# Kernel optimization log

Measured on AMD Instinct MI355X. Metric: run time of the kernel, lower is better.

The kernel has to match this reference:

```python
import jax, jax.numpy as jnp
import numpy as np

B, S, E = 2, 2048, 4096
H, KVH, D = 32, 8, 128
GROUPS = H // KVH
MAX_POS = 4096
ROPE_THETA = 10000.0


def _rope_tables(max_pos, dim, theta):
    inv_freq = 1.0 / (theta ** (jnp.arange(0, dim, 2, dtype=jnp.float32) / dim))
    t = jnp.arange(max_pos, dtype=jnp.float32)
    freqs = jnp.einsum('i,j->ij', t, inv_freq)        # [max_pos, dim/2]
    emb = jnp.concatenate([freqs, freqs], axis=-1)    # [max_pos, dim]
    return jnp.cos(emb), jnp.sin(emb)


def _rotate_half(x):
    x1, x2 = x[..., : x.shape[-1] // 2], x[..., x.shape[-1] // 2:]
    return jnp.concatenate([-x2, x1], axis=-1)


def setup_inputs() -> dict:
    key = jax.random.key(0)
    ks = jax.random.split(key, 8)
    scale_w = 1.0 / np.sqrt(E)
    query = jax.random.normal(ks[0], (B, S, E), dtype=jnp.float32)
    k_in = jax.random.normal(ks[1], (B, S, E), dtype=jnp.float32)
    v_in = jax.random.normal(ks[2], (B, S, E), dtype=jnp.float32)
    position_ids = jnp.broadcast_to(jnp.arange(S, dtype=jnp.int64), (B, S))
    # causal mask: 1 where attending allowed, 0 elsewhere
    src_mask = jnp.tril(jnp.ones((S, S), dtype=jnp.int32))
    src_mask = jnp.broadcast_to(src_mask, (B, S, S))
    Wq = jax.random.normal(ks[3], (E, H * D), dtype=jnp.float32) * scale_w
    Wk = jax.random.normal(ks[4], (E, KVH * D), dtype=jnp.float32) * scale_w
    Wv = jax.random.normal(ks[5], (E, KVH * D), dtype=jnp.float32) * scale_w
    Wo = jax.random.normal(ks[6], (H * D, E), dtype=jnp.float32) * scale_w
    return {"query": query, "key": k_in, "value": v_in,
            "position_ids": position_ids, "src_mask": src_mask,
            "Wq": Wq, "Wk": Wk, "Wv": Wv, "Wo": Wo}


def reference(query, key, value, position_ids, src_mask, Wq, Wk, Wv, Wo):
    nb, q_len, _ = query.shape
    # projections -> [B, heads, S, D]
    q = (query @ Wq).reshape(nb, q_len, H, D).transpose(0, 2, 1, 3)
    k = (key @ Wk).reshape(nb, q_len, KVH, D).transpose(0, 2, 1, 3)
    v = (value @ Wv).reshape(nb, q_len, KVH, D).transpose(0, 2, 1, 3)
    # RoPE
    cos_t, sin_t = _rope_tables(MAX_POS, D, ROPE_THETA)
    cos = cos_t[position_ids][:, None]  # [B,1,S,D]
    sin = sin_t[position_ids][:, None]
    q = q * cos + _rotate_half(q) * sin
    k = k * cos + _rotate_half(k) * sin
    # repeat_kv (interleave groups) -> [B,H,S,D]
    k = jnp.repeat(k, GROUPS, axis=1)
    v = jnp.repeat(v, GROUPS, axis=1)
    # attention core
    scores = jnp.einsum('bhqd,bhkd->bhqk', q, k) / jnp.sqrt(jnp.float32(D))
    mask = src_mask[:, None]  # [B,1,S,S]
    scores = jnp.where(mask == 0, jnp.float32(-1e9), scores)
    attn = jax.nn.softmax(scores, axis=-1)
    x = jnp.einsum('bhqk,bhkd->bhqd', attn, v)
    x = x.transpose(0, 2, 1, 3).reshape(nb, q_len, H * D)
    return x @ Wo
```

## Files before the change

### kernel.cpp

```cpp
#include <hip/hip_runtime.h>
#include <stdint.h>

#define B_ 2
#define S_ 2048
#define E_ 4096
#define H_ 32
#define KVH_ 8
#define D_ 128

typedef __bf16 bf16_t;
typedef __bf16 bf16x8 __attribute__((ext_vector_type(8)));
typedef __bf16 bf16x4 __attribute__((ext_vector_type(4)));
typedef float f32x4 __attribute__((ext_vector_type(4)));

__device__ __forceinline__ void gl2lds16(const void* g, void* l) {
  __builtin_amdgcn_global_load_lds(
      (__attribute__((address_space(1))) void*)(uintptr_t)g,
      (__attribute__((address_space(3))) void*)(uint32_t)(uintptr_t)l,
      16, 0, 0);
}

__global__ void cvt_f32_bf16(const float* __restrict__ in, bf16_t* __restrict__ out, int n4) {
  int i = blockIdx.x * 256 + threadIdx.x;
  if (i < n4) {
    float4 v = ((const float4*)in)[i];
    bf16x4 o;
    o.x = (bf16_t)v.x; o.y = (bf16_t)v.y; o.z = (bf16_t)v.z; o.w = (bf16_t)v.w;
    ((bf16x4*)out)[i] = o;
  }
}

__global__ void transpose_cvt(const float* __restrict__ in, bf16_t* __restrict__ out,
                              int R, int C) {
  __shared__ float t[32][33];
  int r0 = blockIdx.y * 32, c0 = blockIdx.x * 32;
  int tx = threadIdx.x & 31, tg = threadIdx.x >> 5;
#pragma unroll
  for (int k = 0; k < 4; ++k) {
    int r = tg * 4 + k;
    t[r][tx] = in[(long)(r0 + r) * C + c0 + tx];
  }
  __syncthreads();
#pragma unroll
  for (int k = 0; k < 4; ++k) {
    int r = tg * 4 + k;
    out[(long)(c0 + r) * R + r0 + tx] = (bf16_t)t[tx][r];
  }
}

__global__ void transpose_v(const float* __restrict__ Vtmp, bf16_t* __restrict__ Vt) {
  __shared__ float t[32][33];
  int z = blockIdx.z, b = z >> 3, kv = z & 7;
  const float* in = Vtmp + (long)b * S_ * (KVH_ * D_) + kv * D_;
  bf16_t* out = Vt + ((long)(b * KVH_ + kv)) * D_ * S_;
  int s0 = blockIdx.y * 32, d0 = blockIdx.x * 32;
  int tx = threadIdx.x & 31, tg = threadIdx.x >> 5;
#pragma unroll
  for (int k = 0; k < 4; ++k) {
    int r = tg * 4 + k;
    t[r][tx] = in[(long)(s0 + r) * (KVH_ * D_) + d0 + tx];
  }
  __syncthreads();
#pragma unroll
  for (int k = 0; k < 4; ++k) {
    int r = tg * 4 + k;
    out[(long)(d0 + r) * S_ + s0 + tx] = (bf16_t)t[tx][r];
  }
}

__global__ void rope_cvt(const float* __restrict__ T, bf16_t* __restrict__ out,
                         const int* __restrict__ pos, int NH, float scale) {
  long idx = (long)blockIdx.x * 256 + threadIdx.x;
  int j = (int)(idx & 63);
  long t = idx >> 6;
  int s = (int)(t % S_); t /= S_;
  int nh = (int)(t % NH);
  int b = (int)(t / NH);
  long row = ((long)b * S_ + s) * ((long)NH * D_) + (long)nh * D_;
  float x1 = T[row + j];
  float x2 = T[row + j + 64];
  float p = (float)pos[(long)b * S_ + s];
  float inv = expf(-(float)j * (9.210340371976184f / 64.0f));
  float fr = p * inv;
  float c = cosf(fr), sn = sinf(fr);
  long ob = (((long)b * NH + nh) * S_ + s) * D_;
  out[ob + j]      = (bf16_t)((x1 * c - x2 * sn) * scale);
  out[ob + j + 64] = (bf16_t)((x2 * c + x1 * sn) * scale);
}

__global__ __launch_bounds__(256, 2) void gemm_bt(
    const bf16_t* __restrict__ A, const bf16_t* __restrict__ Bt,
    float* __restrict__ C, int M, int N, int K) {
  __shared__ bf16_t As[128 * 64];
  __shared__ bf16_t Bs[128 * 64];
  const int tid = threadIdx.x;
  const int lane = tid & 63;
  const int wave = tid >> 6;
  const int m0 = blockIdx.y * 128, n0 = blockIdx.x * 128;
  const int wm = (wave >> 1) * 64, wn = (wave & 1) * 64;
  const int ln = lane & 15, quad = lane >> 4;
  const int srow = lane >> 3;
  const int sg = lane & 7;

  f32x4 acc[4][4] = {};

  for (int kb = 0; kb < K; kb += 64) {
    __syncthreads();
#pragma unroll
    for (int it = 0; it < 4; ++it) {
      int c = wave * 4 + it;
      int row = c * 8 + srow;
      int g = sg ^ (row & 7);
      gl2lds16(A + (long)(m0 + row) * K + kb + g * 8, &As[c * 512 + lane * 8]);
      gl2lds16(Bt + (long)(n0 + row) * K + kb + g * 8, &Bs[c * 512 + lane * 8]);
    }
    __syncthreads();
#pragma unroll
    for (int ks = 0; ks < 2; ++ks) {
      bf16x8 af[4], bfr[4];
      const int go = ((ks * 4 + quad) ^ (ln & 7)) * 8;
#pragma unroll
      for (int i = 0; i < 4; ++i)
        af[i] = *(const bf16x8*)&As[(wm + i * 16 + ln) * 64 + go];
#pragma unroll
      for (int j = 0; j < 4; ++j)
        bfr[j] = *(const bf16x8*)&Bs[(wn + j * 16 + ln) * 64 + go];
#pragma unroll
      for (int i = 0; i < 4; ++i)
#pragma unroll
        for (int j = 0; j < 4; ++j)
          acc[i][j] = __builtin_amdgcn_mfma_f32_16x16x32_bf16(af[i], bfr[j], acc[i][j], 0, 0, 0);
    }
  }
#pragma unroll
  for (int i = 0; i < 4; ++i)
#pragma unroll
    for (int j = 0; j < 4; ++j)
#pragma unroll
      for (int r = 0; r < 4; ++r) {
        int m = m0 + wm + i * 16 + quad * 4 + r;
        int n = n0 + wn + j * 16 + ln;
        C[(long)m * N + n] = acc[i][j][r];
      }
}

__global__ __launch_bounds__(256, 1) void flash_attn(
    const bf16_t* __restrict__ Q, const bf16_t* __restrict__ Kr,
    const bf16_t* __restrict__ Vt, bf16_t* __restrict__ X) {
  __shared__ bf16_t Plds[4 * 32 * 128];
  const int tid = threadIdx.x, lane = tid & 63, wave = tid >> 6;
  const int ln = lane & 15, quad = lane >> 4;

  const int d = blockIdx.x;
  const int wid = (d & 7) * 128 + (d >> 3);
  const int qi = 15 - (wid & 15);
  const int h = (wid >> 4) & 31;
  const int b = wid >> 9;
  const int kv = h >> 2;
  const bf16_t* Kbase = Kr + (((long)b * KVH_ + kv) * S_) * D_;
  const bf16_t* Vbase = Vt + (((long)b * KVH_ + kv) * D_) * S_;
  bf16_t* Pw = &Plds[wave * 4096];

  bf16x8 aq[2][4];
  {
    const bf16_t* Qw = Q + (((long)b * H_ + h) * S_ + qi * 128 + wave * 32) * D_;
#pragma unroll
    for (int i = 0; i < 2; ++i)
#pragma unroll
      for (int ks = 0; ks < 4; ++ks)
        aq[i][ks] = *(const bf16x8*)(Qw + (i * 16 + ln) * D_ + ks * 32 + quad * 8);
  }

  f32x4 o_acc[2][8] = {};
  float m_cur[2][4], l_cur[2][4];
#pragma unroll
  for (int i = 0; i < 2; ++i)
#pragma unroll
    for (int r = 0; r < 4; ++r) { m_cur[i][r] = -__builtin_inff(); l_cur[i][r] = 0.f; }

  for (int jt = 0; jt <= qi; ++jt) {
    const bf16_t* Kt = Kbase + (long)jt * 128 * D_;

    f32x4 s_acc[2][8] = {};
#pragma unroll
    for (int ks = 0; ks < 4; ++ks) {
      bf16x8 bk[8];
#pragma unroll
      for (int j = 0; j < 8; ++j)
        bk[j] = *(const bf16x8*)(Kt + (long)(j * 16 + ln) * D_ + ks * 32 + quad * 8);
      __builtin_amdgcn_s_setprio(1);
#pragma unroll
      for (int i = 0; i < 2; ++i)
#pragma unroll
        for (int j = 0; j < 8; ++j)
          s_acc[i][j] = __builtin_amdgcn_mfma_f32_16x16x32_bf16(aq[i][ks], bk[j], s_acc[i][j], 0, 0, 0);
      __builtin_amdgcn_s_setprio(0);
    }

#pragma unroll
    for (int i = 0; i < 2; ++i) {
      float rmax[4];
#pragma unroll
      for (int r = 0; r < 4; ++r) rmax[r] = -__builtin_inff();
#pragma unroll
      for (int j = 0; j < 8; ++j)
#pragma unroll
        for (int r = 0; r < 4; ++r) {
          float v = s_acc[i][j][r];
          if (jt == qi) {
            int qrow = wave * 32 + i * 16 + quad * 4 + r;
            int kcol = j * 16 + ln;
            if (kcol > qrow) v = -__builtin_inff();
          }
          s_acc[i][j][r] = v;
          rmax[r] = fmaxf(rmax[r], v);
        }
#pragma unroll
      for (int r = 0; r < 4; ++r) {
        float v = rmax[r];
        v = fmaxf(v, __shfl_xor(v, 1));
        v = fmaxf(v, __shfl_xor(v, 2));
        v = fmaxf(v, __shfl_xor(v, 4));
        v = fmaxf(v, __shfl_xor(v, 8));
        rmax[r] = v;
      }
      float alpha[4];
#pragma unroll
      for (int r = 0; r < 4; ++r) {
        float mn = fmaxf(m_cur[i][r], rmax[r]);
        alpha[r] = exp2f(m_cur[i][r] - mn);
        m_cur[i][r] = mn;
      }
      float rsum[4] = {0.f, 0.f, 0.f, 0.f};
#pragma unroll
      for (int j = 0; j < 8; ++j)
#pragma unroll
        for (int r = 0; r < 4; ++r) {
          float p = exp2f(s_acc[i][j][r] - m_cur[i][r]);
          s_acc[i][j][r] = p;
          rsum[r] += p;
        }
#pragma unroll
      for (int r = 0; r < 4; ++r) {
        float v = rsum[r];
        v += __shfl_xor(v, 1);
        v += __shfl_xor(v, 2);
        v += __shfl_xor(v, 4);
        v += __shfl_xor(v, 8);
        l_cur[i][r] = l_cur[i][r] * alpha[r] + v;
      }
#pragma unroll
      for (int j = 0; j < 8; ++j)
#pragma unroll
        for (int r = 0; r < 4; ++r)
          o_acc[i][j][r] *= alpha[r];
#pragma unroll
      for (int j = 0; j < 8; ++j)
#pragma unroll
        for (int r = 0; r < 4; ++r) {
          int prow = i * 16 + quad * 4 + r;
          int pg = (j * 2 + (ln >> 3)) ^ (prow & 15);
          Pw[prow * 128 + pg * 8 + (ln & 7)] = (bf16_t)s_acc[i][j][r];
        }
    }

#pragma unroll
    for (int ks = 0; ks < 4; ++ks) {
      bf16x8 ap[2], bv[8];
      const int go = ((ks * 4 + quad) ^ ln) * 8;
#pragma unroll
      for (int i = 0; i < 2; ++i)
        ap[i] = *(const bf16x8*)&Pw[(i * 16 + ln) * 128 + go];
#pragma unroll
      for (int j = 0; j < 8; ++j)
        bv[j] = *(const bf16x8*)(Vbase + (long)(j * 16 + ln) * S_ + jt * 128 + ks * 32 + quad * 8);
      __builtin_amdgcn_s_setprio(1);
#pragma unroll
      for (int i = 0; i < 2; ++i)
#pragma unroll
        for (int j = 0; j < 8; ++j)
          o_acc[i][j] = __builtin_amdgcn_mfma_f32_16x16x32_bf16(ap[i], bv[j], o_acc[i][j], 0, 0, 0);
      __builtin_amdgcn_s_setprio(0);
    }
  }

#pragma unroll
  for (int i = 0; i < 2; ++i) {
    float rl[4];
#pragma unroll
    for (int r = 0; r < 4; ++r) rl[r] = 1.0f / l_cur[i][r];
#pragma unroll
    for (int j = 0; j < 8; ++j)
#pragma unroll
      for (int r = 0; r < 4; ++r) {
        int q = qi * 128 + wave * 32 + i * 16 + quad * 4 + r;
        int dcol = j * 16 + ln;
        float o = o_acc[i][j][r] * rl[r];
        X[((long)b * S_ + q) * (H_ * D_) + (long)h * D_ + dcol] = (bf16_t)o;
      }
  }
}

extern "C" void kernel_launch(void* const* d_in, const int* in_sizes, int n_in,
                              void* d_out, int out_size, void* d_ws, size_t ws_size,
                              hipStream_t stream) {
  const float* query = (const float*)d_in[0];
  const float* key   = (const float*)d_in[1];
  const float* value = (const float*)d_in[2];
  const int*   pos   = (const int*)d_in[3];
  const float* Wq = (const float*)d_in[5];
  const float* Wk = (const float*)d_in[6];
  const float* Wv = (const float*)d_in[7];
  const float* Wo = (const float*)d_in[8];
  float* out = (float*)d_out;

  char* ws = (char*)d_ws;
  size_t off = 0;
  auto alloc = [&](size_t bytes) {
    char* p = ws + off;
    off += (bytes + 1023) & ~(size_t)1023;
    return p;
  };
  bf16_t* Wqt = (bf16_t*)alloc(33554432);
  bf16_t* Wkt = (bf16_t*)alloc(8388608);
  bf16_t* Wvt = (bf16_t*)alloc(8388608);
  bf16_t* Wot = (bf16_t*)alloc(33554432);
  bf16_t* Xq  = (bf16_t*)alloc(33554432);
  bf16_t* Xk  = (bf16_t*)alloc(33554432);
  bf16_t* Xv  = (bf16_t*)alloc(33554432);
  float*  Ktmp = (float*)alloc(16777216);
  float*  Vtmp = (float*)alloc(16777216);
  float*  Qtmp = out;
  bf16_t* Qr = Xk;
  bf16_t* Kr = Xv;
  bf16_t* Vt = (bf16_t*)((char*)Xv + 8388608);
  bf16_t* X  = Xq;

  const int n4 = B_ * S_ * E_ / 4;
  cvt_f32_bf16<<<n4 / 256, 256, 0, stream>>>(query, Xq, n4);
  cvt_f32_bf16<<<n4 / 256, 256, 0, stream>>>(key, Xk, n4);
  cvt_f32_bf16<<<n4 / 256, 256, 0, stream>>>(value, Xv, n4);

  transpose_cvt<<<dim3(128, 128), 256, 0, stream>>>(Wq, Wqt, 4096, 4096);
  transpose_cvt<<<dim3(32, 128), 256, 0, stream>>>(Wk, Wkt, 4096, 1024);
  transpose_cvt<<<dim3(32, 128), 256, 0, stream>>>(Wv, Wvt, 4096, 1024);
  transpose_cvt<<<dim3(128, 128), 256, 0, stream>>>(Wo, Wot, 4096, 4096);

  gemm_bt<<<dim3(32, 32), 256, 0, stream>>>(Xq, Wqt, Qtmp, 4096, 4096, 4096);
  gemm_bt<<<dim3(8, 32), 256, 0, stream>>>(Xk, Wkt, Ktmp, 4096, 1024, 4096);
  gemm_bt<<<dim3(8, 32), 256, 0, stream>>>(Xv, Wvt, Vtmp, 4096, 1024, 4096);

  rope_cvt<<<(B_ * H_ * S_ * 64) / 256, 256, 0, stream>>>(Qtmp, Qr, pos, H_, 0.12751743f);
  rope_cvt<<<(B_ * KVH_ * S_ * 64) / 256, 256, 0, stream>>>(Ktmp, Kr, pos, KVH_, 1.0f);
  transpose_v<<<dim3(4, 64, 16), 256, 0, stream>>>(Vtmp, Vt);

  flash_attn<<<dim3(1024), 256, 0, stream>>>(Qr, Kr, Vt, X);

  gemm_bt<<<dim3(32, 32), 256, 0, stream>>>(X, Wot, out, 4096, 4096, 4096);
}
```

Before: 1.252 ms.

## Double-buffer K/V register loads and add lazy softmax rescaling in flash attention

Splits the K and V fragment loads into ping-pong register buffers so global loads for the next k-step (and the next tile's first K slice) are issued while MFMAs on the current slice run. The online softmax now rescales the output and running max only when any lane's row max grows past a threshold of 8 (log2 units), and keeps per-lane partial row sums that are reduced across lanes once at the end, which drops the per-tile shuffle reductions. The cost is higher register pressure from the four fragment buffers, plus a prefetch one tile past the causal end that reads valid but unused memory. The lazy rescale accepts bounded exp growth in exchange for fewer multiplies.

```diff
diff --git a/kernel.cpp b/kernel.cpp
--- a/kernel.cpp
+++ b/kernel.cpp
@@ -161,6 +161,9 @@
   const bf16_t* Vbase = Vt + (((long)b * KVH_ + kv) * D_) * S_;
   bf16_t* Pw = &Plds[wave * 4096];
 
+  const int klo = ln * D_ + quad * 8;
+  const int vlo = ln * S_ + quad * 8;
+
   bf16x8 aq[2][4];
   {
     const bf16_t* Qw = Q + (((long)b * H_ + h) * S_ + qi * 128 + wave * 32) * D_;
@@ -172,30 +175,57 @@
   }
 
   f32x4 o_acc[2][8] = {};
-  float m_cur[2][4], l_cur[2][4];
+  float m_cur[2][4], l_par[2][4];
 #pragma unroll
   for (int i = 0; i < 2; ++i)
 #pragma unroll
-    for (int r = 0; r < 4; ++r) { m_cur[i][r] = -__builtin_inff(); l_cur[i][r] = 0.f; }
+    for (int r = 0; r < 4; ++r) { m_cur[i][r] = -__builtin_inff(); l_par[i][r] = 0.f; }
+
+  bf16x8 bkA[8], bkB[8], bvA[8], bvB[8];
+#pragma unroll
+  for (int j = 0; j < 8; ++j)
+    bkA[j] = *(const bf16x8*)(Kbase + j * 16 * D_ + klo);
 
   for (int jt = 0; jt <= qi; ++jt) {
-    const bf16_t* Kt = Kbase + (long)jt * 128 * D_;
-
+    const int kt = jt * 128 * D_;
+    const int vt0 = jt * 128;
     f32x4 s_acc[2][8] = {};
-#pragma unroll
-    for (int ks = 0; ks < 4; ++ks) {
-      bf16x8 bk[8];
-#pragma unroll
-      for (int j = 0; j < 8; ++j)
-        bk[j] = *(const bf16x8*)(Kt + (long)(j * 16 + ln) * D_ + ks * 32 + quad * 8);
-      __builtin_amdgcn_s_setprio(1);
-#pragma unroll
-      for (int i = 0; i < 2; ++i)
-#pragma unroll
-        for (int j = 0; j < 8; ++j)
-          s_acc[i][j] = __builtin_amdgcn_mfma_f32_16x16x32_bf16(aq[i][ks], bk[j], s_acc[i][j], 0, 0, 0);
-      __builtin_amdgcn_s_setprio(0);
-    }
+
+#pragma unroll
+    for (int j = 0; j < 8; ++j)
+      bkB[j] = *(const bf16x8*)(Kbase + kt + j * 16 * D_ + 32 + klo);
+    __builtin_amdgcn_s_setprio(1);
+#pragma unroll
+    for (int i = 0; i < 2; ++i)
+#pragma unroll
+      for (int j = 0; j < 8; ++j)
+        s_acc[i][j] = __builtin_amdgcn_mfma_f32_16x16x32_bf16(aq[i][0], bkA[j], s_acc[i][j], 0, 0, 0);
+    __builtin_amdgcn_s_setprio(0);
+#pragma unroll
+    for (int j = 0; j < 8; ++j)
+      bkA[j] = *(const bf16x8*)(Kbase + kt + j * 16 * D_ + 64 + klo);
+    __builtin_amdgcn_s_setprio(1);
+#pragma unroll
+    for (int i = 0; i < 2; ++i)
+#pragma unroll
+      for (int j = 0; j < 8; ++j)
+        s_acc[i][j] = __builtin_amdgcn_mfma_f32_16x16x32_bf16(aq[i][1], bkB[j], s_acc[i][j], 0, 0, 0);
+    __builtin_amdgcn_s_setprio(0);
+#pragma unroll
+    for (int j = 0; j < 8; ++j)
+      bkB[j] = *(const bf16x8*)(Kbase + kt + j * 16 * D_ + 96 + klo);
+    __builtin_amdgcn_s_setprio(1);
+#pragma unroll
+    for (int i = 0; i < 2; ++i)
+#pragma unroll
+      for (int j = 0; j < 8; ++j)
+        s_acc[i][j] = __builtin_amdgcn_mfma_f32_16x16x32_bf16(aq[i][2], bkA[j], s_acc[i][j], 0, 0, 0);
+#pragma unroll
+    for (int i = 0; i < 2; ++i)
+#pragma unroll
+      for (int j = 0; j < 8; ++j)
+        s_acc[i][j] = __builtin_amdgcn_mfma_f32_16x16x32_bf16(aq[i][3], bkB[j], s_acc[i][j], 0, 0, 0);
+    __builtin_amdgcn_s_setprio(0);
 
 #pragma unroll
     for (int i = 0; i < 2; ++i) {
@@ -224,36 +254,31 @@
         v = fmaxf(v, __shfl_xor(v, 8));
         rmax[r] = v;
       }
-      float alpha[4];
-#pragma unroll
-      for (int r = 0; r < 4; ++r) {
-        float mn = fmaxf(m_cur[i][r], rmax[r]);
-        alpha[r] = exp2f(m_cur[i][r] - mn);
-        m_cur[i][r] = mn;
+      float grow = fmaxf(fmaxf(rmax[0] - m_cur[i][0], rmax[1] - m_cur[i][1]),
+                         fmaxf(rmax[2] - m_cur[i][2], rmax[3] - m_cur[i][3]));
+      if (__any(grow > 8.0f)) {
+        float alpha[4];
+#pragma unroll
+        for (int r = 0; r < 4; ++r) {
+          float mn = fmaxf(m_cur[i][r], rmax[r]);
+          alpha[r] = exp2f(m_cur[i][r] - mn);
+          m_cur[i][r] = mn;
+          l_par[i][r] *= alpha[r];
+        }
+#pragma unroll
+        for (int j = 0; j < 8; ++j)
+#pragma unroll
+          for (int r = 0; r < 4; ++r)
+            o_acc[i][j][r] *= alpha[r];
       }
-      float rsum[4] = {0.f, 0.f, 0.f, 0.f};
 #pragma unroll
       for (int j = 0; j < 8; ++j)
 #pragma unroll
         for (int r = 0; r < 4; ++r) {
           float p = exp2f(s_acc[i][j][r] - m_cur[i][r]);
           s_acc[i][j][r] = p;
-          rsum[r] += p;
+          l_par[i][r] += p;
         }
-#pragma unroll
-      for (int r = 0; r < 4; ++r) {
-        float v = rsum[r];
-        v += __shfl_xor(v, 1);
-        v += __shfl_xor(v, 2);
-        v += __shfl_xor(v, 4);
-        v += __shfl_xor(v, 8);
-        l_cur[i][r] = l_cur[i][r] * alpha[r] + v;
-      }
-#pragma unroll
-      for (int j = 0; j < 8; ++j)
-#pragma unroll
-        for (int r = 0; r < 4; ++r)
-          o_acc[i][j][r] *= alpha[r];
 #pragma unroll
       for (int j = 0; j < 8; ++j)
 #pragma unroll
@@ -262,24 +287,79 @@
           int pg = (j * 2 + (ln >> 3)) ^ (prow & 15);
           Pw[prow * 128 + pg * 8 + (ln & 7)] = (bf16_t)s_acc[i][j][r];
         }
-    }
-
-#pragma unroll
-    for (int ks = 0; ks < 4; ++ks) {
-      bf16x8 ap[2], bv[8];
-      const int go = ((ks * 4 + quad) ^ ln) * 8;
-#pragma unroll
-      for (int i = 0; i < 2; ++i)
-        ap[i] = *(const bf16x8*)&Pw[(i * 16 + ln) * 128 + go];
-#pragma unroll
-      for (int j = 0; j < 8; ++j)
-        bv[j] = *(const bf16x8*)(Vbase + (long)(j * 16 + ln) * S_ + jt * 128 + ks * 32 + quad * 8);
+      if (i == 0) {
+#pragma unroll
+        for (int j = 0; j < 8; ++j)
+          bvA[j] = *(const bf16x8*)(Vbase + j * 16 * S_ + vt0 + vlo);
+      }
+    }
+
+#pragma unroll
+    for (int j = 0; j < 8; ++j)
+      bvB[j] = *(const bf16x8*)(Vbase + j * 16 * S_ + vt0 + 32 + vlo);
+    {
+      bf16x8 ap[2];
+      const int go0 = (quad ^ ln) * 8;
+#pragma unroll
+      for (int i = 0; i < 2; ++i)
+        ap[i] = *(const bf16x8*)&Pw[(i * 16 + ln) * 128 + go0];
       __builtin_amdgcn_s_setprio(1);
 #pragma unroll
       for (int i = 0; i < 2; ++i)
 #pragma unroll
         for (int j = 0; j < 8; ++j)
-          o_acc[i][j] = __builtin_amdgcn_mfma_f32_16x16x32_bf16(ap[i], bv[j], o_acc[i][j], 0, 0, 0);
+          o_acc[i][j] = __builtin_amdgcn_mfma_f32_16x16x32_bf16(ap[i], bvA[j], o_acc[i][j], 0, 0, 0);
+      __builtin_amdgcn_s_setprio(0);
+    }
+#pragma unroll
+    for (int j = 0; j < 8; ++j)
+      bvA[j] = *(const bf16x8*)(Vbase + j * 16 * S_ + vt0 + 64 + vlo);
+#pragma unroll
+    for (int j = 0; j < 8; ++j)
+      bkA[j] = *(const bf16x8*)(Kbase + kt + 128 * D_ + j * 16 * D_ + klo);
+    {
+      bf16x8 ap[2];
+      const int go1 = ((4 + quad) ^ ln) * 8;
+#pragma unroll
+      for (int i = 0; i < 2; ++i)
+        ap[i] = *(const bf16x8*)&Pw[(i * 16 + ln) * 128 + go1];
+      __builtin_amdgcn_s_setprio(1);
+#pragma unroll
+      for (int i = 0; i < 2; ++i)
+#pragma unroll
+        for (int j = 0; j < 8; ++j)
+          o_acc[i][j] = __builtin_amdgcn_mfma_f32_16x16x32_bf16(ap[i], bvB[j], o_acc[i][j], 0, 0, 0);
+      __builtin_amdgcn_s_setprio(0);
+    }
+#pragma unroll
+    for (int j = 0; j < 8; ++j)
+      bvB[j] = *(const bf16x8*)(Vbase + j * 16 * S_ + vt0 + 96 + vlo);
+    {
+      bf16x8 ap[2];
+      const int go2 = ((8 + quad) ^ ln) * 8;
+#pragma unroll
+      for (int i = 0; i < 2; ++i)
+        ap[i] = *(const bf16x8*)&Pw[(i * 16 + ln) * 128 + go2];
+      __builtin_amdgcn_s_setprio(1);
+#pragma unroll
+      for (int i = 0; i < 2; ++i)
+#pragma unroll
+        for (int j = 0; j < 8; ++j)
+          o_acc[i][j] = __builtin_amdgcn_mfma_f32_16x16x32_bf16(ap[i], bvA[j], o_acc[i][j], 0, 0, 0);
+      __builtin_amdgcn_s_setprio(0);
+    }
+    {
+      bf16x8 ap[2];
+      const int go3 = ((12 + quad) ^ ln) * 8;
+#pragma unroll
+      for (int i = 0; i < 2; ++i)
+        ap[i] = *(const bf16x8*)&Pw[(i * 16 + ln) * 128 + go3];
+      __builtin_amdgcn_s_setprio(1);
+#pragma unroll
+      for (int i = 0; i < 2; ++i)
+#pragma unroll
+        for (int j = 0; j < 8; ++j)
+          o_acc[i][j] = __builtin_amdgcn_mfma_f32_16x16x32_bf16(ap[i], bvB[j], o_acc[i][j], 0, 0, 0);
       __builtin_amdgcn_s_setprio(0);
     }
   }
@@ -288,7 +368,14 @@
   for (int i = 0; i < 2; ++i) {
     float rl[4];
 #pragma unroll
-    for (int r = 0; r < 4; ++r) rl[r] = 1.0f / l_cur[i][r];
+    for (int r = 0; r < 4; ++r) {
+      float lsum = l_par[i][r];
+      lsum += __shfl_xor(lsum, 1);
+      lsum += __shfl_xor(lsum, 2);
+      lsum += __shfl_xor(lsum, 4);
+      lsum += __shfl_xor(lsum, 8);
+      rl[r] = 1.0f / lsum;
+    }
 #pragma unroll
     for (int j = 0; j < 8; ++j)
 #pragma unroll
```

Result: no change. 1.235 ms (-1.3%).

## Restructure flash attention with LDS-staged K/V triple buffering and lazy rescaling

Applied to the files above, without the earlier changes.

The attention kernel now uses 512-thread blocks that cover 256 query rows and walk 64-wide KV tiles. K and V tiles are loaded asynchronously into swizzled LDS with a three-deep global_load_lds pipeline and shared by all eight waves, instead of each wave reading K/V straight from global memory. It also skips the softmax rescale unless the running max grows by more than a threshold, and defers the row-sum reduction to the end. The costs are more barriers per tile, idle waves on causal-tail tiles, and a larger LDS footprint.

```diff
diff --git a/kernel.cpp b/kernel.cpp
--- a/kernel.cpp
+++ b/kernel.cpp
@@ -144,143 +144,174 @@
       }
 }
 
-__global__ __launch_bounds__(256, 1) void flash_attn(
+#define QBLK_ 256
+#define KVBLK_ 64
+__global__ __launch_bounds__(512, 1) void flash_attn(
     const bf16_t* __restrict__ Q, const bf16_t* __restrict__ Kr,
     const bf16_t* __restrict__ Vt, bf16_t* __restrict__ X) {
-  __shared__ bf16_t Plds[4 * 32 * 128];
+  __shared__ bf16_t Ks[3][KVBLK_ * D_];
+  __shared__ bf16_t Vs[3][D_ * KVBLK_];
+  __shared__ bf16_t Plds[8][32 * KVBLK_];
   const int tid = threadIdx.x, lane = tid & 63, wave = tid >> 6;
   const int ln = lane & 15, quad = lane >> 4;
 
   const int d = blockIdx.x;
-  const int wid = (d & 7) * 128 + (d >> 3);
-  const int qi = 15 - (wid & 15);
-  const int h = (wid >> 4) & 31;
-  const int b = wid >> 9;
+  const int wid = (d & 7) * 64 + (d >> 3);
+  const int qb = 7 - (wid & 7);
+  const int h = (wid >> 3) & 31;
+  const int b = wid >> 8;
   const int kv = h >> 2;
   const bf16_t* Kbase = Kr + (((long)b * KVH_ + kv) * S_) * D_;
   const bf16_t* Vbase = Vt + (((long)b * KVH_ + kv) * D_) * S_;
-  bf16_t* Pw = &Plds[wave * 4096];
+  bf16_t* Pw = Plds[wave];
+
+  const int nt = 4 * qb + 4;
+  const int jlast = 4 * qb + (wave >> 1);
 
   bf16x8 aq[2][4];
   {
-    const bf16_t* Qw = Q + (((long)b * H_ + h) * S_ + qi * 128 + wave * 32) * D_;
+    const bf16_t* Qw = Q + (((long)b * H_ + h) * S_ + qb * QBLK_ + wave * 32) * D_;
 #pragma unroll
     for (int i = 0; i < 2; ++i)
 #pragma unroll
       for (int ks = 0; ks < 4; ++ks)
         aq[i][ks] = *(const bf16x8*)(Qw + (i * 16 + ln) * D_ + ks * 32 + quad * 8);
   }
+  asm volatile("s_waitcnt vmcnt(0)" ::: "memory");
+
+  auto STAGE = [&](int bi, int jt) {
+    const bf16_t* Kt = Kbase + (long)jt * KVBLK_ * D_;
+    const int vcol = jt * KVBLK_;
+#pragma unroll
+    for (int it = 0; it < 2; ++it) {
+      int c = wave * 2 + it;
+      int krow = c * 4 + quad;
+      int kg = ln ^ (krow & 15);
+      gl2lds16(Kt + krow * D_ + kg * 8, &Ks[bi][c * 512 + lane * 8]);
+      int vrow = c * 8 + (lane >> 3);
+      int vg = (lane & 7) ^ (vrow & 7);
+      gl2lds16(Vbase + (long)vrow * S_ + vcol + vg * 8, &Vs[bi][c * 512 + lane * 8]);
+    }
+  };
 
   f32x4 o_acc[2][8] = {};
-  float m_cur[2][4], l_cur[2][4];
+  float m_cur[2][4], l_par[2][4];
 #pragma unroll
   for (int i = 0; i < 2; ++i)
 #pragma unroll
-    for (int r = 0; r < 4; ++r) { m_cur[i][r] = -__builtin_inff(); l_cur[i][r] = 0.f; }
-
-  for (int jt = 0; jt <= qi; ++jt) {
-    const bf16_t* Kt = Kbase + (long)jt * 128 * D_;
-
-    f32x4 s_acc[2][8] = {};
-#pragma unroll
-    for (int ks = 0; ks < 4; ++ks) {
-      bf16x8 bk[8];
-#pragma unroll
-      for (int j = 0; j < 8; ++j)
-        bk[j] = *(const bf16x8*)(Kt + (long)(j * 16 + ln) * D_ + ks * 32 + quad * 8);
-      __builtin_amdgcn_s_setprio(1);
-#pragma unroll
-      for (int i = 0; i < 2; ++i)
+    for (int r = 0; r < 4; ++r) { m_cur[i][r] = -__builtin_inff(); l_par[i][r] = 0.f; }
+
+  STAGE(0, 0);
+  STAGE(1, 1);
+
+  for (int jt = 0; jt < nt; ++jt) {
+    if (jt < nt - 1) asm volatile("s_waitcnt vmcnt(4)" ::: "memory");
+    else             asm volatile("s_waitcnt vmcnt(0)" ::: "memory");
+    __builtin_amdgcn_s_barrier();
+    __builtin_amdgcn_sched_barrier(0);
+    if (jt + 2 < nt) STAGE((jt + 2) % 3, jt + 2);
+
+    if (jt <= jlast) {
+      const bf16_t* Kb = Ks[jt % 3];
+      const bf16_t* Vb = Vs[jt % 3];
+
+      f32x4 s_acc[2][4] = {};
+#pragma unroll
+      for (int ks = 0; ks < 4; ++ks) {
+        bf16x8 bk[4];
+        const int go = ((ks * 4 + quad) ^ ln) * 8;
+#pragma unroll
+        for (int j = 0; j < 4; ++j)
+          bk[j] = *(const bf16x8*)&Kb[(j * 16 + ln) * D_ + go];
+        __builtin_amdgcn_s_setprio(1);
+#pragma unroll
+        for (int i = 0; i < 2; ++i)
+#pragma unroll
+          for (int j = 0; j < 4; ++j)
+            s_acc[i][j] = __builtin_amdgcn_mfma_f32_16x16x32_bf16(aq[i][ks], bk[j], s_acc[i][j], 0, 0, 0);
+        __builtin_amdgcn_s_setprio(0);
+      }
+
+#pragma unroll
+      for (int i = 0; i < 2; ++i) {
+        float rmax[4];
+#pragma unroll
+        for (int r = 0; r < 4; ++r) rmax[r] = -__builtin_inff();
+#pragma unroll
+        for (int j = 0; j < 4; ++j)
+#pragma unroll
+          for (int r = 0; r < 4; ++r) {
+            float v = s_acc[i][j][r];
+            if (jt == jlast) {
+              int qrow = qb * QBLK_ + wave * 32 + i * 16 + quad * 4 + r;
+              int kcol = jt * KVBLK_ + j * 16 + ln;
+              if (kcol > qrow) v = -__builtin_inff();
+            }
+            s_acc[i][j][r] = v;
+            rmax[r] = fmaxf(rmax[r], v);
+          }
+#pragma unroll
+        for (int r = 0; r < 4; ++r) {
+          float v = rmax[r];
+          v = fmaxf(v, __shfl_xor(v, 1));
+          v = fmaxf(v, __shfl_xor(v, 2));
+          v = fmaxf(v, __shfl_xor(v, 4));
+          v = fmaxf(v, __shfl_xor(v, 8));
+          rmax[r] = v;
+        }
+        float grow = fmaxf(fmaxf(rmax[0] - m_cur[i][0], rmax[1] - m_cur[i][1]),
+                           fmaxf(rmax[2] - m_cur[i][2], rmax[3] - m_cur[i][3]));
+        if (__any(grow > 8.0f)) {
+          float alpha[4];
+#pragma unroll
+          for (int r = 0; r < 4; ++r) {
+            float mn = fmaxf(m_cur[i][r], rmax[r]);
+            alpha[r] = exp2f(m_cur[i][r] - mn);
+            m_cur[i][r] = mn;
+            l_par[i][r] *= alpha[r];
+          }
+#pragma unroll
+          for (int j = 0; j < 8; ++j)
+#pragma unroll
+            for (int r = 0; r < 4; ++r)
+              o_acc[i][j][r] *= alpha[r];
+        }
+#pragma unroll
+        for (int j = 0; j < 4; ++j)
+#pragma unroll
+          for (int r = 0; r < 4; ++r) {
+            float p = exp2f(s_acc[i][j][r] - m_cur[i][r]);
+            s_acc[i][j][r] = p;
+            l_par[i][r] += p;
+          }
+#pragma unroll
+        for (int j = 0; j < 4; ++j)
+#pragma unroll
+          for (int r = 0; r < 4; ++r) {
+            int prow = i * 16 + quad * 4 + r;
+            int pg = (j * 2 + (ln >> 3)) ^ (prow & 7);
+            Pw[prow * KVBLK_ + pg * 8 + (ln & 7)] = (bf16_t)s_acc[i][j][r];
+          }
+      }
+
+#pragma unroll
+      for (int ks = 0; ks < 2; ++ks) {
+        bf16x8 ap[2], bv[8];
+        const int go = ((ks * 4 + quad) ^ (ln & 7)) * 8;
+#pragma unroll
+        for (int i = 0; i < 2; ++i)
+          ap[i] = *(const bf16x8*)&Pw[(i * 16 + ln) * KVBLK_ + go];
 #pragma unroll
         for (int j = 0; j < 8; ++j)
-          s_acc[i][j] = __builtin_amdgcn_mfma_f32_16x16x32_bf16(aq[i][ks], bk[j], s_acc[i][j], 0, 0, 0);
-      __builtin_amdgcn_s_setprio(0);
-    }
-
-#pragma unroll
-    for (int i = 0; i < 2; ++i) {
-      float rmax[4];
-#pragma unroll
-      for (int r = 0; r < 4; ++r) rmax[r] = -__builtin_inff();
-#pragma unroll
-      for (int j = 0; j < 8; ++j)
-#pragma unroll
-        for (int r = 0; r < 4; ++r) {
-          float v = s_acc[i][j][r];
-          if (jt == qi) {
-            int qrow = wave * 32 + i * 16 + quad * 4 + r;
-            int kcol = j * 16 + ln;
-            if (kcol > qrow) v = -__builtin_inff();
-          }
-          s_acc[i][j][r] = v;
-          rmax[r] = fmaxf(rmax[r], v);
-        }
-#pragma unroll
-      for (int r = 0; r < 4; ++r) {
-        float v = rmax[r];
-        v = fmaxf(v, __shfl_xor(v, 1));
-        v = fmaxf(v, __shfl_xor(v, 2));
-        v = fmaxf(v, __shfl_xor(v, 4));
-        v = fmaxf(v, __shfl_xor(v, 8));
-        rmax[r] = v;
-      }
-      float alpha[4];
-#pragma unroll
-      for (int r = 0; r < 4; ++r) {
-        float mn = fmaxf(m_cur[i][r], rmax[r]);
-        alpha[r] = exp2f(m_cur[i][r] - mn);
-        m_cur[i][r] = mn;
-      }
-      float rsum[4] = {0.f, 0.f, 0.f, 0.f};
-#pragma unroll
-      for (int j = 0; j < 8; ++j)
-#pragma unroll
-        for (int r = 0; r < 4; ++r) {
-          float p = exp2f(s_acc[i][j][r] - m_cur[i][r]);
-          s_acc[i][j][r] = p;
-          rsum[r] += p;
-        }
-#pragma unroll
-      for (int r = 0; r < 4; ++r) {
-        float v = rsum[r];
-        v += __shfl_xor(v, 1);
-        v += __shfl_xor(v, 2);
-        v += __shfl_xor(v, 4);
-        v += __shfl_xor(v, 8);
-        l_cur[i][r] = l_cur[i][r] * alpha[r] + v;
-      }
-#pragma unroll
-      for (int j = 0; j < 8; ++j)
-#pragma unroll
-        for (int r = 0; r < 4; ++r)
-          o_acc[i][j][r] *= alpha[r];
-#pragma unroll
-      for (int j = 0; j < 8; ++j)
-#pragma unroll
-        for (int r = 0; r < 4; ++r) {
-          int prow = i * 16 + quad * 4 + r;
-          int pg = (j * 2 + (ln >> 3)) ^ (prow & 15);
-          Pw[prow * 128 + pg * 8 + (ln & 7)] = (bf16_t)s_acc[i][j][r];
-        }
-    }
-
-#pragma unroll
-    for (int ks = 0; ks < 4; ++ks) {
-      bf16x8 ap[2], bv[8];
-      const int go = ((ks * 4 + quad) ^ ln) * 8;
-#pragma unroll
-      for (int i = 0; i < 2; ++i)
-        ap[i] = *(const bf16x8*)&Pw[(i * 16 + ln) * 128 + go];
-#pragma unroll
-      for (int j = 0; j < 8; ++j)
-        bv[j] = *(const bf16x8*)(Vbase + (long)(j * 16 + ln) * S_ + jt * 128 + ks * 32 + quad * 8);
-      __builtin_amdgcn_s_setprio(1);
-#pragma unroll
-      for (int i = 0; i < 2; ++i)
-#pragma unroll
-        for (int j = 0; j < 8; ++j)
-          o_acc[i][j] = __builtin_amdgcn_mfma_f32_16x16x32_bf16(ap[i], bv[j], o_acc[i][j], 0, 0, 0);
-      __builtin_amdgcn_s_setprio(0);
+          bv[j] = *(const bf16x8*)&Vb[(j * 16 + ln) * KVBLK_ + go];
+        __builtin_amdgcn_s_setprio(1);
+#pragma unroll
+        for (int i = 0; i < 2; ++i)
+#pragma unroll
+          for (int j = 0; j < 8; ++j)
+            o_acc[i][j] = __builtin_amdgcn_mfma_f32_16x16x32_bf16(ap[i], bv[j], o_acc[i][j], 0, 0, 0);
+        __builtin_amdgcn_s_setprio(0);
+      }
     }
   }
 
@@ -288,12 +319,19 @@
   for (int i = 0; i < 2; ++i) {
     float rl[4];
 #pragma unroll
-    for (int r = 0; r < 4; ++r) rl[r] = 1.0f / l_cur[i][r];
+    for (int r = 0; r < 4; ++r) {
+      float lsum = l_par[i][r];
+      lsum += __shfl_xor(lsum, 1);
+      lsum += __shfl_xor(lsum, 2);
+      lsum += __shfl_xor(lsum, 4);
+      lsum += __shfl_xor(lsum, 8);
+      rl[r] = 1.0f / lsum;
+    }
 #pragma unroll
     for (int j = 0; j < 8; ++j)
 #pragma unroll
       for (int r = 0; r < 4; ++r) {
-        int q = qi * 128 + wave * 32 + i * 16 + quad * 4 + r;
+        int q = qb * QBLK_ + wave * 32 + i * 16 + quad * 4 + r;
         int dcol = j * 16 + ln;
         float o = o_acc[i][j][r] * rl[r];
         X[((long)b * S_ + q) * (H_ * D_) + (long)h * D_ + dcol] = (bf16_t)o;
@@ -354,7 +392,7 @@
   rope_cvt<<<(B_ * KVH_ * S_ * 64) / 256, 256, 0, stream>>>(Ktmp, Kr, pos, KVH_, 1.0f);
   transpose_v<<<dim3(4, 64, 16), 256, 0, stream>>>(Vtmp, Vt);
 
-  flash_attn<<<dim3(1024), 256, 0, stream>>>(Qr, Kr, Vt, X);
+  flash_attn<<<dim3(512), 512, 0, stream>>>(Qr, Kr, Vt, X);
 
   gemm_bt<<<dim3(32, 32), 256, 0, stream>>>(X, Wot, out, 4096, 4096, 4096);
 }
```

New measurement: 1.116 ms. 10.8% less time.
